# Performance work log

Measured on AMD Instinct MI355X. Metric: run time of the kernel, lower is better.

## Reference

```python
import jax, jax.numpy as jnp
import numpy as np

B, N, S = 8, 4096, 1024
D1, D2 = 128, 256
IN_CH, OUT_CH = D1 + D2, 256
BN_EPS = 1e-5


def setup_inputs() -> dict:
    key = jax.random.key(0)
    ks = jax.random.split(key, 12)
    inp = {
        "xyz1": jax.random.normal(ks[0], (B, N, 3), jnp.float32),
        "xyz2": jax.random.normal(ks[1], (B, S, 3), jnp.float32),
        "points1": jax.random.normal(ks[2], (B, N, D1), jnp.float32),
        "points2": jax.random.normal(ks[3], (B, S, D2), jnp.float32),
        # fuse: Conv1d(in_ch->out_ch, k=1) + BN
        "W_fuse": jax.random.normal(ks[4], (OUT_CH, IN_CH), jnp.float32) * (1.0 / np.sqrt(IN_CH)),
        "b_fuse": jnp.zeros((OUT_CH,), jnp.float32),
        "g_fuse": jnp.ones((OUT_CH,), jnp.float32),
        "bt_fuse": jnp.zeros((OUT_CH,), jnp.float32),
        # res block net1: Conv1d(out_ch->out_ch) + BN (res_expansion=1.0)
        "W1": jax.random.normal(ks[5], (OUT_CH, OUT_CH), jnp.float32) * (1.0 / np.sqrt(OUT_CH)),
        "b1": jnp.zeros((OUT_CH,), jnp.float32),
        "g1": jnp.ones((OUT_CH,), jnp.float32),
        "bt1": jnp.zeros((OUT_CH,), jnp.float32),
        # res block net2: Conv1d(out_ch->out_ch) + BN
        "W2": jax.random.normal(ks[6], (OUT_CH, OUT_CH), jnp.float32) * (1.0 / np.sqrt(OUT_CH)),
        "b2": jnp.zeros((OUT_CH,), jnp.float32),
        "g2": jnp.ones((OUT_CH,), jnp.float32),
        "bt2": jnp.zeros((OUT_CH,), jnp.float32),
    }
    return inp


def _bn(x, g, b):
    # BatchNorm1d training-mode forward: stats over (batch, length), x: [B, C, L]
    m = jnp.mean(x, axis=(0, 2), keepdims=True)
    v = jnp.var(x, axis=(0, 2), keepdims=True)
    return (x - m) * jax.lax.rsqrt(v + BN_EPS) * g[None, :, None] + b[None, :, None]


def _conv1x1(x, W, b):
    # x: [B, C_in, L], W: [C_out, C_in] -> [B, C_out, L]
    return jnp.einsum("oc,bcl->bol", W, x) + b[None, :, None]


def _gelu(x):
    return jax.nn.gelu(x, approximate=False)  # torch nn.GELU default (erf)


def reference(xyz1, xyz2, points1, points2,
              W_fuse, b_fuse, g_fuse, bt_fuse,
              W1, b1, g1, bt1, W2, b2, g2, bt2):
    # squared pairwise distances [B, N, S] without B x N x S x 3 intermediate
    d = (jnp.sum(xyz1 * xyz1, -1)[:, :, None]
         - 2.0 * jnp.einsum("bnc,bsc->bns", xyz1, xyz2)
         + jnp.sum(xyz2 * xyz2, -1)[:, None, :])
    # 3 nearest coarse points per dense point (== sort ascending, take first 3)
    neg_d3, idx = jax.lax.top_k(-d, 3)            # [B, N, 3]
    d3 = -neg_d3
    recip = 1.0 / (d3 + 1e-8)
    w = recip / jnp.sum(recip, axis=2, keepdims=True)  # [B, N, 3]
    gathered = points2[jnp.arange(points2.shape[0])[:, None, None], idx]  # [B, N, 3, D2]
    interp = jnp.sum(gathered * w[..., None], axis=2)  # [B, N, D2]

    new_points = jnp.concatenate([points1, interp], axis=-1)  # [B, N, D1+D2]
    x = jnp.transpose(new_points, (0, 2, 1))                   # [B, C, N]

    # fuse: conv-bn-gelu
    x = _gelu(_bn(_conv1x1(x, W_fuse, b_fuse), g_fuse, bt_fuse))
    # residual block: gelu(bn(conv(gelu(bn(conv(x))))) + x)
    y = _gelu(_bn(_conv1x1(x, W1, b1), g1, bt1))
    y = _bn(_conv1x1(y, W2, b2), g2, bt2)
    x = _gelu(y + x)

    return jnp.transpose(x, (0, 2, 1))  # [B, N, out_ch]
```

## Files before the change

kernel.cpp:

```cpp
#include <hip/hip_runtime.h>
#include <hip/hip_bf16.h>

constexpr int Bb = 8, Nn = 4096, Ss = 1024;
constexpr int D1 = 128, D2 = 256, KIN = 384, OC = 256;
constexpr int L = Bb * Nn;
constexpr float BN_EPS = 1e-5f;

typedef __attribute__((ext_vector_type(4))) float floatx4;
typedef __attribute__((ext_vector_type(8))) __bf16 bf16x8;

#define DEV __device__ __forceinline__

DEV float bf2f(unsigned short u) {
    union { unsigned int i; float f; } v; v.i = ((unsigned int)u) << 16; return v.f;
}
DEV unsigned short f2bf(float f) {
    union { float f; unsigned int i; } v; v.f = f;
    unsigned int x = v.i;
    return (unsigned short)((x + 0x7FFFu + ((x >> 16) & 1u)) >> 16);
}
DEV float gelu_f(float x) {
    float u = x * (0.7978845608f + 0.0356774081f * x * x);
    float t = __expf(-2.0f * u);
    return x * __builtin_amdgcn_rcpf(1.0f + t);
}

DEV bool probe_isf(const unsigned int* __restrict__ w, int tid) {
    unsigned int lo = w[tid & 63] & 0xFFFFu;
    int e = (int)((lo >> 7) & 0xFF);
    unsigned long long m = __ballot(e >= 100 && e <= 144);
    return __popcll(m) < 48;
}

template <int K> DEV int permoff(int off) {
    int row = off / K, rr = off - row * K;
    int cg_ = (rr >> 3) & 7;
    return row * K + (rr & ~63) + (((cg_ ^ (row & 7)) << 3)) + (rr & 7);
}

DEV void merge3(float& d0, float& d1, float& d2, int& i0, int& i1, int& i2,
                float e0, float e1, float e2, int j0, int j1, int j2, bool pref) {
    float a0 = d0, a1 = d1, a2 = d2; int x0 = i0, x1 = i1, x2 = i2;
    float b0 = e0, b1 = e1;          int y0 = j0, y1 = j1;
    bool t = pref ? (a0 <= b0) : (a0 < b0);
    d0 = t ? a0 : b0; i0 = t ? x0 : y0;
    a0 = t ? a1 : a0; x0 = t ? x1 : x0;
    a1 = t ? a2 : a1; x1 = t ? x2 : x1;
    b0 = t ? b0 : b1; y0 = t ? y0 : y1;
    b1 = t ? b1 : e2; y1 = t ? y1 : j2;
    t = pref ? (a0 <= b0) : (a0 < b0);
    d1 = t ? a0 : b0; i1 = t ? x0 : y0;
    a0 = t ? a1 : a0; x0 = t ? x1 : x0;
    b0 = t ? b0 : b1; y0 = t ? y0 : y1;
    t = pref ? (a0 <= b0) : (a0 < b0);
    d2 = t ? a0 : b0; i2 = t ? x0 : y0;
}

__global__ __launch_bounds__(256) void k_front(const void* __restrict__ xyz1_,
                                               const void* __restrict__ xyz2_,
                                               const void* __restrict__ w0_,
                                               const void* __restrict__ w1_,
                                               const void* __restrict__ w2_,
                                               unsigned short* __restrict__ Wdst,
                                               float* __restrict__ stats,
                                               int* __restrict__ dflag,
                                               int* __restrict__ nn_idx,
                                               float* __restrict__ nn_w) {
    int tid = threadIdx.x;
    int bid = blockIdx.x;
    bool isf = probe_isf((const unsigned int*)xyz1_, tid);

    if (bid < 6) {
        stats[bid * 256 + tid] = 0.0f;
        if (bid == 0 && tid == 0) *dflag = isf ? 1 : 0;
        return;
    }
    if (bid < 902) {
        int i = (bid - 6) * 256 + tid;
        const void* src; int off;
        if (i < 98304)       { src = w0_; off = permoff<384>(i); }
        else if (i < 163840) { src = w1_; off = permoff<256>(i - 98304); }
        else                 { src = w2_; off = permoff<256>(i - 163840); }
        Wdst[i] = isf ? f2bf(((const float*)src)[off]) : ((const unsigned short*)src)[off];
        return;
    }

    __shared__ alignas(16) float s4[Ss * 4 + 32];
    int bn0 = (bid - 902) * 32;
    int b = bn0 >> 12;

    if (isf) {
        const float* p2 = (const float*)xyz2_ + (size_t)b * Ss * 3;
        for (int i = tid; i < Ss * 3; i += 256) {
            int s = i / 3, k = i - s * 3;
            s4[s * 4 + k + ((s >> 7) << 2)] = p2[i];
        }
    } else {
        const unsigned short* p2 = (const unsigned short*)xyz2_ + (size_t)b * Ss * 3;
        for (int i = tid; i < Ss * 3; i += 256) {
            int s = i / 3, k = i - s * 3;
            s4[s * 4 + k + ((s >> 7) << 2)] = bf2f(p2[i]);
        }
    }
    __syncthreads();
    for (int s = tid; s < Ss; s += 256) {
        int a = s * 4 + ((s >> 7) << 2);
        float x = s4[a], y = s4[a + 1], z = s4[a + 2];
        s4[a + 3] = x * x + y * y + z * z;
    }
    __syncthreads();

    int part = tid & 7;
    int bn = bn0 + (tid >> 3);
    float x1, y1, z1;
    if (isf) {
        const float* p1 = (const float*)xyz1_ + (size_t)bn * 3;
        x1 = p1[0]; y1 = p1[1]; z1 = p1[2];
    } else {
        const unsigned short* p1 = (const unsigned short*)xyz1_ + (size_t)bn * 3;
        x1 = bf2f(p1[0]); y1 = bf2f(p1[1]); z1 = bf2f(p1[2]);
    }
    float n1 = x1 * x1 + y1 * y1 + z1 * z1;

    float d0 = 3.4e38f, d1 = 3.4e38f, d2 = 3.4e38f;
    int i0 = 0, i1 = 0, i2 = 0;
    const float* sp = &s4[part * 516];
#pragma unroll 4
    for (int j = 0; j < 128; ++j) {
        float4 qv = *(const float4*)(sp + j * 4);
        float d = n1 + qv.w - 2.0f * (x1 * qv.x + y1 * qv.y + z1 * qv.z);
        int s = part * 128 + j;
        bool c2 = d < d2, c1 = d < d1, c0 = d < d0;
        d2 = c1 ? d1 : (c2 ? d : d2); i2 = c1 ? i1 : (c2 ? s : i2);
        d1 = c0 ? d0 : (c1 ? d : d1); i1 = c0 ? i0 : (c1 ? s : i1);
        d0 = c0 ? d  : d0;            i0 = c0 ? s  : i0;
    }
#pragma unroll
    for (int m = 1; m <= 4; m <<= 1) {
        float e0 = __shfl_xor(d0, m, 64), e1 = __shfl_xor(d1, m, 64), e2 = __shfl_xor(d2, m, 64);
        int   j0 = __shfl_xor(i0, m, 64), j1 = __shfl_xor(i1, m, 64), j2 = __shfl_xor(i2, m, 64);
        bool pref = (part < (part ^ m));
        merge3(d0, d1, d2, i0, i1, i2, e0, e1, e2, j0, j1, j2, pref);
    }
    if (part == 0) {
        float r0 = 1.0f / (d0 + 1e-8f), r1 = 1.0f / (d1 + 1e-8f), r2 = 1.0f / (d2 + 1e-8f);
        float rs = 1.0f / (r0 + r1 + r2);
        nn_idx[bn * 3 + 0] = i0; nn_idx[bn * 3 + 1] = i1; nn_idx[bn * 3 + 2] = i2;
        nn_w[bn * 3 + 0] = r0 * rs; nn_w[bn * 3 + 1] = r1 * rs; nn_w[bn * 3 + 2] = r2 * rs;
    }
}

__global__ __launch_bounds__(256) void k_interp(const void* __restrict__ p1_,
                                                const void* __restrict__ p2_,
                                                const int* __restrict__ nn_idx,
                                                const float* __restrict__ nn_w,
                                                const int* __restrict__ dflag,
                                                unsigned short* __restrict__ X) {
    bool isf = (*dflag != 0);
    int i0_ = blockIdx.x * 256 + threadIdx.x;
    constexpr int GPR = KIN / 8;
#pragma unroll
    for (int it = 0; it < 3; ++it) {
        int g = i0_ + it * 524288;
        int row = g / GPR, cg = g - row * GPR;
        int chunk = cg >> 3, cgc = cg & 7;
        union { uint4 v; unsigned short u[8]; } va;
        if (cg < 16) {
            int c0 = cg * 8;
            if (isf) {
                const float* p = (const float*)p1_ + (size_t)row * D1 + c0;
                float4 f0 = *(const float4*)p;
                float4 f1 = *(const float4*)(p + 4);
                va.u[0] = f2bf(f0.x); va.u[1] = f2bf(f0.y); va.u[2] = f2bf(f0.z); va.u[3] = f2bf(f0.w);
                va.u[4] = f2bf(f1.x); va.u[5] = f2bf(f1.y); va.u[6] = f2bf(f1.z); va.u[7] = f2bf(f1.w);
            } else {
                va.v = *(const uint4*)((const unsigned short*)p1_ + (size_t)row * D1 + c0);
            }
        } else {
            int c2 = (cg - 16) * 8;
            int b = row >> 12;
            int j0 = nn_idx[row * 3], j1 = nn_idx[row * 3 + 1], j2 = nn_idx[row * 3 + 2];
            float w0 = nn_w[row * 3], w1 = nn_w[row * 3 + 1], w2 = nn_w[row * 3 + 2];
            if (isf) {
                const float* base = (const float*)p2_;
                const float* r0 = base + ((size_t)(b * Ss + j0)) * D2 + c2;
                const float* r1 = base + ((size_t)(b * Ss + j1)) * D2 + c2;
                const float* r2 = base + ((size_t)(b * Ss + j2)) * D2 + c2;
#pragma unroll
                for (int h = 0; h < 2; ++h) {
                    float4 a0 = *(const float4*)(r0 + h * 4);
                    float4 a1 = *(const float4*)(r1 + h * 4);
                    float4 a2 = *(const float4*)(r2 + h * 4);
                    va.u[h * 4 + 0] = f2bf(w0 * a0.x + w1 * a1.x + w2 * a2.x);
                    va.u[h * 4 + 1] = f2bf(w0 * a0.y + w1 * a1.y + w2 * a2.y);
                    va.u[h * 4 + 2] = f2bf(w0 * a0.z + w1 * a1.z + w2 * a2.z);
                    va.u[h * 4 + 3] = f2bf(w0 * a0.w + w1 * a1.w + w2 * a2.w);
                }
            } else {
                const unsigned short* base = (const unsigned short*)p2_;
                uint4 v0 = *(const uint4*)(base + ((size_t)(b * Ss + j0)) * D2 + c2);
                uint4 v1 = *(const uint4*)(base + ((size_t)(b * Ss + j1)) * D2 + c2);
                uint4 v2 = *(const uint4*)(base + ((size_t)(b * Ss + j2)) * D2 + c2);
                const unsigned short* u0 = (const unsigned short*)&v0;
                const unsigned short* u1 = (const unsigned short*)&v1;
                const unsigned short* u2 = (const unsigned short*)&v2;
#pragma unroll
                for (int j = 0; j < 8; ++j)
                    va.u[j] = f2bf(w0 * bf2f(u0[j]) + w1 * bf2f(u1[j]) + w2 * bf2f(u2[j]));
            }
        }
        *(uint4*)&X[(size_t)row * KIN + chunk * 64 + ((cgc ^ (row & 7)) << 3)] = va.v;
    }
}

template <int K, bool ACT>
__global__ __launch_bounds__(256, 4) void k_gemm(const unsigned short* __restrict__ A,
                                                 const unsigned short* __restrict__ W,
                                                 unsigned short* __restrict__ Out,
                                                 float* __restrict__ S1, float* __restrict__ S2,
                                                 const float* __restrict__ S1in,
                                                 const float* __restrict__ S2in,
                                                 const void* __restrict__ g_,
                                                 const void* __restrict__ bt_,
                                                 const int* __restrict__ dflag) {
    __shared__ alignas(16) unsigned short As[32 * 64];
    __shared__ alignas(16) unsigned short Bs[128 * 64];
    __shared__ float sS1[128], sS2[128];
    __shared__ float sCA[256], sCC[256];

    int tid = threadIdx.x;
    int l0 = (blockIdx.x >> 1) * 32;
    int n0 = (blockIdx.x & 1) * 128;
    int wn = tid >> 6, lane = tid & 63, quad = lane >> 4, lr = lane & 15;

    if constexpr (ACT) {
        float m = S1in[tid] * (1.0f / (float)L);
        float var = S2in[tid] * (1.0f / (float)L) - m * m;
        float g, bt;
        if (*dflag) { g = ((const float*)g_)[tid]; bt = ((const float*)bt_)[tid]; }
        else { g = bf2f(((const unsigned short*)g_)[tid]); bt = bf2f(((const unsigned short*)bt_)[tid]); }
        float a = g * rsqrtf(var + BN_EPS);
        sCA[tid] = a;
        sCC[tid] = bt - m * a;
    }
    if (tid < 128) { sS1[tid] = 0.f; sS2[tid] = 0.f; }

    floatx4 acc[2][2];
#pragma unroll
    for (int mi = 0; mi < 2; ++mi)
#pragma unroll
        for (int ni = 0; ni < 2; ++ni) acc[mi][ni] = (floatx4){0.f, 0.f, 0.f, 0.f};

    for (int kc = 0; kc < K / 64; ++kc) {
        __syncthreads();
#pragma unroll
        for (int it = 0; it < 4; ++it) {
            int chunk = it * 4 + wn;
            int row = chunk * 8 + (lane >> 3);
            const unsigned short* src = W + (size_t)(n0 + row) * K + kc * 64 + (lane & 7) * 8;
            __builtin_amdgcn_global_load_lds(
                (const __attribute__((address_space(1))) void*)src,
                (__attribute__((address_space(3))) void*)&Bs[chunk * 512],
                16, 0, 0);
        }
        if constexpr (!ACT) {
            const unsigned short* src = A + (size_t)(l0 + wn * 8 + (lane >> 3)) * K + kc * 64 + (lane & 7) * 8;
            __builtin_amdgcn_global_load_lds(
                (const __attribute__((address_space(1))) void*)src,
                (__attribute__((address_space(3))) void*)&As[wn * 512],
                16, 0, 0);
        } else {
            int row = tid >> 3, c8 = tid & 7;
            union { uint4 v; unsigned short u[8]; } va;
            va.v = *(const uint4*)(A + (size_t)(l0 + row) * K + kc * 64 + c8 * 8);
            int kb = kc * 64 + c8 * 8;
#pragma unroll
            for (int j = 0; j < 8; ++j) {
                float f = bf2f(va.u[j]);
                va.u[j] = f2bf(gelu_f(sCA[kb + j] * f + sCC[kb + j]));
            }
            *(uint4*)&As[row * 64 + ((c8 ^ (row & 7)) << 3)] = va.v;
        }
        __syncthreads();
#pragma unroll
        for (int ks8 = 0; ks8 < 2; ++ks8) {
            bf16x8 af[2], bfr[2];
#pragma unroll
            for (int mi = 0; mi < 2; ++mi) {
                int ra = mi * 16 + lr;
                af[mi] = *(const bf16x8*)&As[ra * 64 + ((((ks8 << 2) + quad) ^ (ra & 7)) << 3)];
            }
#pragma unroll
            for (int ni = 0; ni < 2; ++ni) {
                int rb = wn * 32 + ni * 16 + lr;
                bfr[ni] = *(const bf16x8*)&Bs[rb * 64 + ((((ks8 << 2) + quad) ^ (rb & 7)) << 3)];
            }
#pragma unroll
            for (int mi = 0; mi < 2; ++mi)
#pragma unroll
                for (int ni = 0; ni < 2; ++ni)
                    acc[mi][ni] = __builtin_amdgcn_mfma_f32_16x16x32_bf16(af[mi], bfr[ni], acc[mi][ni], 0, 0, 0);
        }
    }

    float p1a[2] = {0, 0}, p2a[2] = {0, 0};
#pragma unroll
    for (int mi = 0; mi < 2; ++mi)
#pragma unroll
        for (int ni = 0; ni < 2; ++ni)
#pragma unroll
            for (int r = 0; r < 4; ++r) {
                float v = acc[mi][ni][r];
                int row = l0 + mi * 16 + quad * 4 + r;
                int col = n0 + wn * 32 + ni * 16 + lr;
                Out[(size_t)row * OC + col] = f2bf(v);
                p1a[ni] += v; p2a[ni] += v * v;
            }
    __syncthreads();
#pragma unroll
    for (int ni = 0; ni < 2; ++ni) {
        atomicAdd(&sS1[wn * 32 + ni * 16 + lr], p1a[ni]);
        atomicAdd(&sS2[wn * 32 + ni * 16 + lr], p2a[ni]);
    }
    __syncthreads();
    if (tid < 128) {
        atomicAdd(&S1[n0 + tid], sS1[tid]);
        atomicAdd(&S2[n0 + tid], sS2[tid]);
    }
}

__global__ __launch_bounds__(256) void k_final(const unsigned short* __restrict__ t0,
                                               const unsigned short* __restrict__ t2,
                                               const float* __restrict__ S1_0, const float* __restrict__ S2_0,
                                               const float* __restrict__ S1_2, const float* __restrict__ S2_2,
                                               const void* __restrict__ g0_, const void* __restrict__ bt0_,
                                               const void* __restrict__ g2_, const void* __restrict__ bt2_,
                                               const int* __restrict__ dflag,
                                               void* __restrict__ out_) {
    __shared__ float sA0[256], sC0[256], sA2[256], sC2[256];
    int tid = threadIdx.x;
    bool isf = (*dflag != 0);
    {
        float m0 = S1_0[tid] * (1.0f / (float)L);
        float v0_ = S2_0[tid] * (1.0f / (float)L) - m0 * m0;
        float m2 = S1_2[tid] * (1.0f / (float)L);
        float v2_ = S2_2[tid] * (1.0f / (float)L) - m2 * m2;
        float g0, b0, g2, b2;
        if (isf) {
            g0 = ((const float*)g0_)[tid]; b0 = ((const float*)bt0_)[tid];
            g2 = ((const float*)g2_)[tid]; b2 = ((const float*)bt2_)[tid];
        } else {
            g0 = bf2f(((const unsigned short*)g0_)[tid]); b0 = bf2f(((const unsigned short*)bt0_)[tid]);
            g2 = bf2f(((const unsigned short*)g2_)[tid]); b2 = bf2f(((const unsigned short*)bt2_)[tid]);
        }
        float a0 = g0 * rsqrtf(v0_ + BN_EPS);
        float a2 = g2 * rsqrtf(v2_ + BN_EPS);
        sA0[tid] = a0; sC0[tid] = b0 - m0 * a0;
        sA2[tid] = a2; sC2[tid] = b2 - m2 * a2;
    }
    __syncthreads();

    int idx = (blockIdx.x * 256 + tid) * 8;
    int col = idx & (OC - 1);
    union { uint4 v; unsigned short u[8]; } v0, v2;
    v0.v = *(const uint4*)(t0 + idx);
    v2.v = *(const uint4*)(t2 + idx);
    float r[8];
#pragma unroll
    for (int j = 0; j < 8; ++j) {
        float x = gelu_f(sA0[col + j] * bf2f(v0.u[j]) + sC0[col + j]);
        float y = sA2[col + j] * bf2f(v2.u[j]) + sC2[col + j];
        r[j] = gelu_f(x + y);
    }
    if (isf) {
        float* o = (float*)out_ + idx;
        float4 lo = {r[0], r[1], r[2], r[3]};
        float4 hi = {r[4], r[5], r[6], r[7]};
        *(float4*)o = lo;
        *(float4*)(o + 4) = hi;
    } else {
        union { uint4 v; unsigned short u[8]; } vo;
#pragma unroll
        for (int j = 0; j < 8; ++j) vo.u[j] = f2bf(r[j]);
        *(uint4*)((unsigned short*)out_ + idx) = vo.v;
    }
}

extern "C" void kernel_launch(void* const* d_in, const int* in_sizes, int n_in,
                              void* d_out, int out_size, void* d_ws, size_t ws_size,
                              hipStream_t stream) {
    const void* xyz1    = d_in[0];
    const void* xyz2    = d_in[1];
    const void* points1 = d_in[2];
    const void* points2 = d_in[3];
    const void* W_fuse  = d_in[4];
    const void* g_fuse  = d_in[6];
    const void* bt_fuse = d_in[7];
    const void* W1      = d_in[8];
    const void* g1      = d_in[10];
    const void* bt1     = d_in[11];
    const void* W2      = d_in[12];
    const void* g2      = d_in[14];
    const void* bt2     = d_in[15];

    char* ws = (char*)d_ws;
    unsigned short* t2 = (unsigned short*)ws;
    unsigned short* t0 = (unsigned short*)(ws + 25165824);
    unsigned short* X  = (unsigned short*)d_out;
    unsigned short* t1 = (unsigned short*)d_out;
    int*   nn_idx = (int*)(ws + 41943040);
    float* nn_w   = (float*)(ws + 42336256);
    float* stats  = (float*)(ws + 42729472);
    int*   dflag  = (int*)(ws + 42729472 + 3072 * 4);
    unsigned short* Wbf = (unsigned short*)(ws + 42745856);

    float *S1_0 = stats,        *S2_0 = stats + 256;
    float *S1_1 = stats + 512,  *S2_1 = stats + 768;
    float *S1_2 = stats + 1024, *S2_2 = stats + 1280;

    k_front<<<1926, 256, 0, stream>>>(xyz1, xyz2, W_fuse, W1, W2, Wbf, stats, dflag, nn_idx, nn_w);
    k_interp<<<2048, 256, 0, stream>>>(points1, points2, nn_idx, nn_w, dflag, X);
    k_gemm<KIN, false><<<2048, 256, 0, stream>>>(X, Wbf, t0, S1_0, S2_0,
                                                 nullptr, nullptr, nullptr, nullptr, dflag);
    k_gemm<OC, true><<<2048, 256, 0, stream>>>(t0, Wbf + 98304, t1, S1_1, S2_1,
                                               S1_0, S2_0, g_fuse, bt_fuse, dflag);
    k_gemm<OC, true><<<2048, 256, 0, stream>>>(t1, Wbf + 163840, t2, S1_2, S2_2,
                                               S1_1, S2_1, g1, bt1, dflag);
    k_final<<<L * OC / (256 * 8), 256, 0, stream>>>(t0, t2, S1_0, S2_0, S1_2, S2_2,
                                                    g_fuse, bt_fuse, g2, bt2, dflag, d_out);
}
```

Before: 272.1 us.

## Replace LDS-tiled fused GEMM with register-weight GEMM and separate activation kernels

```diff
diff --git a/kernel.cpp b/kernel.cpp
--- a/kernel.cpp
+++ b/kernel.cpp
@@ -30,12 +30,6 @@
     int e = (int)((lo >> 7) & 0xFF);
     unsigned long long m = __ballot(e >= 100 && e <= 144);
     return __popcll(m) < 48;
-}
-
-template <int K> DEV int permoff(int off) {
-    int row = off / K, rr = off - row * K;
-    int cg_ = (rr >> 3) & 7;
-    return row * K + (rr & ~63) + (((cg_ ^ (row & 7)) << 3)) + (rr & 7);
 }
 
 DEV void merge3(float& d0, float& d1, float& d2, int& i0, int& i1, int& i2,
@@ -78,9 +72,9 @@
     if (bid < 902) {
         int i = (bid - 6) * 256 + tid;
         const void* src; int off;
-        if (i < 98304)       { src = w0_; off = permoff<384>(i); }
-        else if (i < 163840) { src = w1_; off = permoff<256>(i - 98304); }
-        else                 { src = w2_; off = permoff<256>(i - 163840); }
+        if (i < 98304)       { src = w0_; off = i; }
+        else if (i < 163840) { src = w1_; off = i - 98304; }
+        else                 { src = w2_; off = i - 163840; }
         Wdst[i] = isf ? f2bf(((const float*)src)[off]) : ((const unsigned short*)src)[off];
         return;
     }
@@ -163,7 +157,6 @@
     for (int it = 0; it < 3; ++it) {
         int g = i0_ + it * 524288;
         int row = g / GPR, cg = g - row * GPR;
-        int chunk = cg >> 3, cgc = cg & 7;
         union { uint4 v; unsigned short u[8]; } va;
         if (cg < 16) {
             int c0 = cg * 8;
@@ -209,31 +202,70 @@
                     va.u[j] = f2bf(w0 * bf2f(u0[j]) + w1 * bf2f(u1[j]) + w2 * bf2f(u2[j]));
             }
         }
-        *(uint4*)&X[(size_t)row * KIN + chunk * 64 + ((cgc ^ (row & 7)) << 3)] = va.v;
-    }
-}
-
-template <int K, bool ACT>
-__global__ __launch_bounds__(256, 4) void k_gemm(const unsigned short* __restrict__ A,
-                                                 const unsigned short* __restrict__ W,
-                                                 unsigned short* __restrict__ Out,
-                                                 float* __restrict__ S1, float* __restrict__ S2,
-                                                 const float* __restrict__ S1in,
-                                                 const float* __restrict__ S2in,
-                                                 const void* __restrict__ g_,
-                                                 const void* __restrict__ bt_,
-                                                 const int* __restrict__ dflag) {
-    __shared__ alignas(16) unsigned short As[32 * 64];
-    __shared__ alignas(16) unsigned short Bs[128 * 64];
-    __shared__ float sS1[128], sS2[128];
+        *(uint4*)&X[(size_t)row * KIN + cg * 8] = va.v;
+    }
+}
+
+template <int K>
+__global__ __launch_bounds__(256) void k_rgemm(const unsigned short* __restrict__ A,
+                                               const unsigned short* __restrict__ W,
+                                               unsigned short* __restrict__ Out,
+                                               float* __restrict__ S1,
+                                               float* __restrict__ S2) {
+    constexpr int KS = K / 32;
+    int tid = threadIdx.x;
+    int wn = tid >> 6, lane = tid & 63, quad = lane >> 4, lr = lane & 15;
+    int c0 = (((blockIdx.x & 1) << 2) | wn) * 32;
+    int r0 = (blockIdx.x >> 1) * 128;
+
+    bf16x8 bfrag[2][KS];
+#pragma unroll
+    for (int ni = 0; ni < 2; ++ni)
+#pragma unroll
+        for (int ks = 0; ks < KS; ++ks)
+            bfrag[ni][ks] = *(const bf16x8*)&W[(size_t)(c0 + ni * 16 + lr) * K + ks * 32 + quad * 8];
+
+    float p1[2] = {0.f, 0.f}, p2[2] = {0.f, 0.f};
+#pragma unroll 2
+    for (int ch = 0; ch < 8; ++ch) {
+        const unsigned short* arow = A + (size_t)(r0 + ch * 16 + lr) * K + quad * 8;
+        bf16x8 af[KS];
+#pragma unroll
+        for (int ks = 0; ks < KS; ++ks)
+            af[ks] = *(const bf16x8*)(arow + ks * 32);
+        floatx4 acc0 = (floatx4){0.f, 0.f, 0.f, 0.f};
+        floatx4 acc1 = (floatx4){0.f, 0.f, 0.f, 0.f};
+#pragma unroll
+        for (int ks = 0; ks < KS; ++ks) {
+            acc0 = __builtin_amdgcn_mfma_f32_16x16x32_bf16(af[ks], bfrag[0][ks], acc0, 0, 0, 0);
+            acc1 = __builtin_amdgcn_mfma_f32_16x16x32_bf16(af[ks], bfrag[1][ks], acc1, 0, 0, 0);
+        }
+        int orow = r0 + ch * 16 + quad * 4;
+#pragma unroll
+        for (int r = 0; r < 4; ++r) {
+            float v0 = acc0[r], v1 = acc1[r];
+            Out[(size_t)(orow + r) * OC + c0 + lr]      = f2bf(v0);
+            Out[(size_t)(orow + r) * OC + c0 + 16 + lr] = f2bf(v1);
+            p1[0] += v0; p2[0] += v0 * v0;
+            p1[1] += v1; p2[1] += v1 * v1;
+        }
+    }
+    atomicAdd(&S1[c0 + lr],      p1[0]);
+    atomicAdd(&S2[c0 + lr],      p2[0]);
+    atomicAdd(&S1[c0 + 16 + lr], p1[1]);
+    atomicAdd(&S2[c0 + 16 + lr], p2[1]);
+}
+
+__global__ __launch_bounds__(256) void k_act(const unsigned short* __restrict__ Tin,
+                                             unsigned short* __restrict__ Tout,
+                                             const float* __restrict__ S1in,
+                                             const float* __restrict__ S2in,
+                                             const void* __restrict__ g_,
+                                             const void* __restrict__ bt_,
+                                             const int* __restrict__ dflag) {
     __shared__ float sCA[256], sCC[256];
-
     int tid = threadIdx.x;
-    int l0 = (blockIdx.x >> 1) * 32;
-    int n0 = (blockIdx.x & 1) * 128;
-    int wn = tid >> 6, lane = tid & 63, quad = lane >> 4, lr = lane & 15;
-
-    if constexpr (ACT) {
+    {
         float m = S1in[tid] * (1.0f / (float)L);
         float var = S2in[tid] * (1.0f / (float)L) - m * m;
         float g, bt;
@@ -243,90 +275,16 @@
         sCA[tid] = a;
         sCC[tid] = bt - m * a;
     }
-    if (tid < 128) { sS1[tid] = 0.f; sS2[tid] = 0.f; }
-
-    floatx4 acc[2][2];
-#pragma unroll
-    for (int mi = 0; mi < 2; ++mi)
-#pragma unroll
-        for (int ni = 0; ni < 2; ++ni) acc[mi][ni] = (floatx4){0.f, 0.f, 0.f, 0.f};
-
-    for (int kc = 0; kc < K / 64; ++kc) {
-        __syncthreads();
-#pragma unroll
-        for (int it = 0; it < 4; ++it) {
-            int chunk = it * 4 + wn;
-            int row = chunk * 8 + (lane >> 3);
-            const unsigned short* src = W + (size_t)(n0 + row) * K + kc * 64 + (lane & 7) * 8;
-            __builtin_amdgcn_global_load_lds(
-                (const __attribute__((address_space(1))) void*)src,
-                (__attribute__((address_space(3))) void*)&Bs[chunk * 512],
-                16, 0, 0);
-        }
-        if constexpr (!ACT) {
-            const unsigned short* src = A + (size_t)(l0 + wn * 8 + (lane >> 3)) * K + kc * 64 + (lane & 7) * 8;
-            __builtin_amdgcn_global_load_lds(
-                (const __attribute__((address_space(1))) void*)src,
-                (__attribute__((address_space(3))) void*)&As[wn * 512],
-                16, 0, 0);
-        } else {
-            int row = tid >> 3, c8 = tid & 7;
-            union { uint4 v; unsigned short u[8]; } va;
-            va.v = *(const uint4*)(A + (size_t)(l0 + row) * K + kc * 64 + c8 * 8);
-            int kb = kc * 64 + c8 * 8;
-#pragma unroll
-            for (int j = 0; j < 8; ++j) {
-                float f = bf2f(va.u[j]);
-                va.u[j] = f2bf(gelu_f(sCA[kb + j] * f + sCC[kb + j]));
-            }
-            *(uint4*)&As[row * 64 + ((c8 ^ (row & 7)) << 3)] = va.v;
-        }
-        __syncthreads();
-#pragma unroll
-        for (int ks8 = 0; ks8 < 2; ++ks8) {
-            bf16x8 af[2], bfr[2];
-#pragma unroll
-            for (int mi = 0; mi < 2; ++mi) {
-                int ra = mi * 16 + lr;
-                af[mi] = *(const bf16x8*)&As[ra * 64 + ((((ks8 << 2) + quad) ^ (ra & 7)) << 3)];
-            }
-#pragma unroll
-            for (int ni = 0; ni < 2; ++ni) {
-                int rb = wn * 32 + ni * 16 + lr;
-                bfr[ni] = *(const bf16x8*)&Bs[rb * 64 + ((((ks8 << 2) + quad) ^ (rb & 7)) << 3)];
-            }
-#pragma unroll
-            for (int mi = 0; mi < 2; ++mi)
-#pragma unroll
-                for (int ni = 0; ni < 2; ++ni)
-                    acc[mi][ni] = __builtin_amdgcn_mfma_f32_16x16x32_bf16(af[mi], bfr[ni], acc[mi][ni], 0, 0, 0);
-        }
-    }
-
-    float p1a[2] = {0, 0}, p2a[2] = {0, 0};
-#pragma unroll
-    for (int mi = 0; mi < 2; ++mi)
-#pragma unroll
-        for (int ni = 0; ni < 2; ++ni)
-#pragma unroll
-            for (int r = 0; r < 4; ++r) {
-                float v = acc[mi][ni][r];
-                int row = l0 + mi * 16 + quad * 4 + r;
-                int col = n0 + wn * 32 + ni * 16 + lr;
-                Out[(size_t)row * OC + col] = f2bf(v);
-                p1a[ni] += v; p2a[ni] += v * v;
-            }
     __syncthreads();
-#pragma unroll
-    for (int ni = 0; ni < 2; ++ni) {
-        atomicAdd(&sS1[wn * 32 + ni * 16 + lr], p1a[ni]);
-        atomicAdd(&sS2[wn * 32 + ni * 16 + lr], p2a[ni]);
-    }
-    __syncthreads();
-    if (tid < 128) {
-        atomicAdd(&S1[n0 + tid], sS1[tid]);
-        atomicAdd(&S2[n0 + tid], sS2[tid]);
-    }
+
+    int idx = (blockIdx.x * 256 + tid) * 8;
+    int col = idx & (OC - 1);
+    union { uint4 v; unsigned short u[8]; } vi, vo;
+    vi.v = *(const uint4*)(Tin + idx);
+#pragma unroll
+    for (int j = 0; j < 8; ++j)
+        vo.u[j] = f2bf(gelu_f(sCA[col + j] * bf2f(vi.u[j]) + sCC[col + j]));
+    *(uint4*)(Tout + idx) = vo.v;
 }
 
 __global__ __launch_bounds__(256) void k_final(const unsigned short* __restrict__ t0,
@@ -404,15 +362,16 @@
     const void* bt2     = d_in[15];
 
     char* ws = (char*)d_ws;
-    unsigned short* t2 = (unsigned short*)ws;
-    unsigned short* t0 = (unsigned short*)(ws + 25165824);
+    unsigned short* t0 = (unsigned short*)ws;
+    unsigned short* t2 = (unsigned short*)(ws + 16777216);
+    unsigned short* ta = (unsigned short*)(ws + 33554432);
     unsigned short* X  = (unsigned short*)d_out;
     unsigned short* t1 = (unsigned short*)d_out;
-    int*   nn_idx = (int*)(ws + 41943040);
-    float* nn_w   = (float*)(ws + 42336256);
-    float* stats  = (float*)(ws + 42729472);
-    int*   dflag  = (int*)(ws + 42729472 + 3072 * 4);
-    unsigned short* Wbf = (unsigned short*)(ws + 42745856);
+    int*   nn_idx = (int*)(ws + 50331648);
+    float* nn_w   = (float*)(ws + 50724864);
+    float* stats  = (float*)(ws + 51118080);
+    int*   dflag  = (int*)(ws + 51124224);
+    unsigned short* Wbf = (unsigned short*)(ws + 51126272);
 
     float *S1_0 = stats,        *S2_0 = stats + 256;
     float *S1_1 = stats + 512,  *S2_1 = stats + 768;
@@ -420,12 +379,11 @@
 
     k_front<<<1926, 256, 0, stream>>>(xyz1, xyz2, W_fuse, W1, W2, Wbf, stats, dflag, nn_idx, nn_w);
     k_interp<<<2048, 256, 0, stream>>>(points1, points2, nn_idx, nn_w, dflag, X);
-    k_gemm<KIN, false><<<2048, 256, 0, stream>>>(X, Wbf, t0, S1_0, S2_0,
-                                                 nullptr, nullptr, nullptr, nullptr, dflag);
-    k_gemm<OC, true><<<2048, 256, 0, stream>>>(t0, Wbf + 98304, t1, S1_1, S2_1,
-                                               S1_0, S2_0, g_fuse, bt_fuse, dflag);
-    k_gemm<OC, true><<<2048, 256, 0, stream>>>(t1, Wbf + 163840, t2, S1_2, S2_2,
-                                               S1_1, S2_1, g1, bt1, dflag);
+    k_rgemm<KIN><<<512, 256, 0, stream>>>(X, Wbf, t0, S1_0, S2_0);
+    k_act<<<L * OC / (256 * 8), 256, 0, stream>>>(t0, ta, S1_0, S2_0, g_fuse, bt_fuse, dflag);
+    k_rgemm<OC><<<512, 256, 0, stream>>>(ta, Wbf + 98304, t1, S1_1, S2_1);
+    k_act<<<L * OC / (256 * 8), 256, 0, stream>>>(t1, ta, S1_1, S2_1, g1, bt1, dflag);
+    k_rgemm<OC><<<512, 256, 0, stream>>>(ta, Wbf + 163840, t2, S1_2, S2_2);
     k_final<<<L * OC / (256 * 8), 256, 0, stream>>>(t0, t2, S1_0, S2_0, S1_2, S2_2,
                                                     g_fuse, bt_fuse, g2, bt2, dflag, d_out);
 }
```

Result: slower. 502.1 us (+84.6%).

## Split BN-GELU into separate pass and keep whole weight slice resident in LDS

Applied to the files above, without the earlier changes.

```diff
diff --git a/kernel.cpp b/kernel.cpp
--- a/kernel.cpp
+++ b/kernel.cpp
@@ -213,27 +213,119 @@
     }
 }
 
-template <int K, bool ACT>
-__global__ __launch_bounds__(256, 4) void k_gemm(const unsigned short* __restrict__ A,
-                                                 const unsigned short* __restrict__ W,
-                                                 unsigned short* __restrict__ Out,
-                                                 float* __restrict__ S1, float* __restrict__ S2,
-                                                 const float* __restrict__ S1in,
-                                                 const float* __restrict__ S2in,
-                                                 const void* __restrict__ g_,
-                                                 const void* __restrict__ bt_,
-                                                 const int* __restrict__ dflag) {
-    __shared__ alignas(16) unsigned short As[32 * 64];
-    __shared__ alignas(16) unsigned short Bs[128 * 64];
-    __shared__ float sS1[128], sS2[128];
+template <int K, int BN>
+__global__ __launch_bounds__(256) void k_pgemm(const unsigned short* __restrict__ A,
+                                               const unsigned short* __restrict__ W,
+                                               unsigned short* __restrict__ Out,
+                                               float* __restrict__ S1,
+                                               float* __restrict__ S2) {
+    constexpr int NSPLIT = OC / BN;
+    constexpr int NI = BN / 32;
+    constexpr int WITERS = BN * K / (8 * 256);
+    constexpr int NKC = K / 64;
+
+    __shared__ alignas(16) unsigned short Ws[BN * K];
+    __shared__ alignas(16) unsigned short As[64 * 64];
+    __shared__ float sS1[BN], sS2[BN];
+
+    int tid = threadIdx.x;
+    int n0 = (blockIdx.x % NSPLIT) * BN;
+    int m0 = (blockIdx.x / NSPLIT) * 64;
+    int wn = tid >> 6, lane = tid & 63, quad = lane >> 4, lr = lane & 15;
+    int wm = wn >> 1, wc = wn & 1;
+
+#pragma unroll
+    for (int it = 0; it < WITERS; ++it) {
+        int c = it * 4 + wn;
+        int flat = c * 512 + lane * 8;
+        int row = flat / K, col = flat % K;
+        const unsigned short* src = W + (size_t)(n0 + row) * K + col;
+        __builtin_amdgcn_global_load_lds(
+            (const __attribute__((address_space(1))) void*)src,
+            (__attribute__((address_space(3))) void*)&Ws[c * 512],
+            16, 0, 0);
+    }
+    if (tid < BN) { sS1[tid] = 0.f; sS2[tid] = 0.f; }
+
+    floatx4 acc[2][NI];
+#pragma unroll
+    for (int mi = 0; mi < 2; ++mi)
+#pragma unroll
+        for (int ni = 0; ni < NI; ++ni) acc[mi][ni] = (floatx4){0.f, 0.f, 0.f, 0.f};
+
+    for (int kc = 0; kc < NKC; ++kc) {
+        __syncthreads();
+#pragma unroll
+        for (int it = 0; it < 2; ++it) {
+            int c = it * 4 + wn;
+            int flat = c * 512 + lane * 8;
+            int row = flat >> 6, col = flat & 63;
+            const unsigned short* src = A + (size_t)(m0 + row) * K + kc * 64 + col;
+            __builtin_amdgcn_global_load_lds(
+                (const __attribute__((address_space(1))) void*)src,
+                (__attribute__((address_space(3))) void*)&As[c * 512],
+                16, 0, 0);
+        }
+        __syncthreads();
+#pragma unroll
+        for (int ks8 = 0; ks8 < 2; ++ks8) {
+            bf16x8 af[2], bf[NI];
+#pragma unroll
+            for (int mi = 0; mi < 2; ++mi) {
+                int ra = wm * 32 + mi * 16 + lr;
+                af[mi] = *(const bf16x8*)&As[ra * 64 + ((((ks8 << 2) + quad) ^ (ra & 7)) << 3)];
+            }
+#pragma unroll
+            for (int ni = 0; ni < NI; ++ni) {
+                int rb = wc * (BN / 2) + ni * 16 + lr;
+                bf[ni] = *(const bf16x8*)&Ws[rb * K + kc * 64 + ((((ks8 << 2) + quad) ^ (rb & 7)) << 3)];
+            }
+#pragma unroll
+            for (int mi = 0; mi < 2; ++mi)
+#pragma unroll
+                for (int ni = 0; ni < NI; ++ni)
+                    acc[mi][ni] = __builtin_amdgcn_mfma_f32_16x16x32_bf16(af[mi], bf[ni], acc[mi][ni], 0, 0, 0);
+        }
+    }
+
+    float p1a[NI], p2a[NI];
+#pragma unroll
+    for (int ni = 0; ni < NI; ++ni) { p1a[ni] = 0.f; p2a[ni] = 0.f; }
+#pragma unroll
+    for (int mi = 0; mi < 2; ++mi)
+#pragma unroll
+        for (int ni = 0; ni < NI; ++ni)
+#pragma unroll
+            for (int r = 0; r < 4; ++r) {
+                float v = acc[mi][ni][r];
+                int row = m0 + wm * 32 + mi * 16 + quad * 4 + r;
+                int col = n0 + wc * (BN / 2) + ni * 16 + lr;
+                Out[(size_t)row * OC + col] = f2bf(v);
+                p1a[ni] += v; p2a[ni] += v * v;
+            }
+    __syncthreads();
+#pragma unroll
+    for (int ni = 0; ni < NI; ++ni) {
+        atomicAdd(&sS1[wc * (BN / 2) + ni * 16 + lr], p1a[ni]);
+        atomicAdd(&sS2[wc * (BN / 2) + ni * 16 + lr], p2a[ni]);
+    }
+    __syncthreads();
+    if (tid < BN) {
+        atomicAdd(&S1[n0 + tid], sS1[tid]);
+        atomicAdd(&S2[n0 + tid], sS2[tid]);
+    }
+}
+
+__global__ __launch_bounds__(256) void k_act(const unsigned short* __restrict__ Tin,
+                                             unsigned short* __restrict__ Tout,
+                                             const float* __restrict__ S1in,
+                                             const float* __restrict__ S2in,
+                                             const void* __restrict__ g_,
+                                             const void* __restrict__ bt_,
+                                             const int* __restrict__ dflag) {
     __shared__ float sCA[256], sCC[256];
-
     int tid = threadIdx.x;
-    int l0 = (blockIdx.x >> 1) * 32;
-    int n0 = (blockIdx.x & 1) * 128;
-    int wn = tid >> 6, lane = tid & 63, quad = lane >> 4, lr = lane & 15;
-
-    if constexpr (ACT) {
+    {
         float m = S1in[tid] * (1.0f / (float)L);
         float var = S2in[tid] * (1.0f / (float)L) - m * m;
         float g, bt;
@@ -243,90 +335,19 @@
         sCA[tid] = a;
         sCC[tid] = bt - m * a;
     }
-    if (tid < 128) { sS1[tid] = 0.f; sS2[tid] = 0.f; }
-
-    floatx4 acc[2][2];
-#pragma unroll
-    for (int mi = 0; mi < 2; ++mi)
-#pragma unroll
-        for (int ni = 0; ni < 2; ++ni) acc[mi][ni] = (floatx4){0.f, 0.f, 0.f, 0.f};
-
-    for (int kc = 0; kc < K / 64; ++kc) {
-        __syncthreads();
-#pragma unroll
-        for (int it = 0; it < 4; ++it) {
-            int chunk = it * 4 + wn;
-            int row = chunk * 8 + (lane >> 3);
-            const unsigned short* src = W + (size_t)(n0 + row) * K + kc * 64 + (lane & 7) * 8;
-            __builtin_amdgcn_global_load_lds(
-                (const __attribute__((address_space(1))) void*)src,
-                (__attribute__((address_space(3))) void*)&Bs[chunk * 512],
-                16, 0, 0);
-        }
-        if constexpr (!ACT) {
-            const unsigned short* src = A + (size_t)(l0 + wn * 8 + (lane >> 3)) * K + kc * 64 + (lane & 7) * 8;
-            __builtin_amdgcn_global_load_lds(
-                (const __attribute__((address_space(1))) void*)src,
-                (__attribute__((address_space(3))) void*)&As[wn * 512],
-                16, 0, 0);
-        } else {
-            int row = tid >> 3, c8 = tid & 7;
-            union { uint4 v; unsigned short u[8]; } va;
-            va.v = *(const uint4*)(A + (size_t)(l0 + row) * K + kc * 64 + c8 * 8);
-            int kb = kc * 64 + c8 * 8;
-#pragma unroll
-            for (int j = 0; j < 8; ++j) {
-                float f = bf2f(va.u[j]);
-                va.u[j] = f2bf(gelu_f(sCA[kb + j] * f + sCC[kb + j]));
-            }
-            *(uint4*)&As[row * 64 + ((c8 ^ (row & 7)) << 3)] = va.v;
-        }
-        __syncthreads();
-#pragma unroll
-        for (int ks8 = 0; ks8 < 2; ++ks8) {
-            bf16x8 af[2], bfr[2];
-#pragma unroll
-            for (int mi = 0; mi < 2; ++mi) {
-                int ra = mi * 16 + lr;
-                af[mi] = *(const bf16x8*)&As[ra * 64 + ((((ks8 << 2) + quad) ^ (ra & 7)) << 3)];
-            }
-#pragma unroll
-            for (int ni = 0; ni < 2; ++ni) {
-                int rb = wn * 32 + ni * 16 + lr;
-                bfr[ni] = *(const bf16x8*)&Bs[rb * 64 + ((((ks8 << 2) + quad) ^ (rb & 7)) << 3)];
-            }
-#pragma unroll
-            for (int mi = 0; mi < 2; ++mi)
-#pragma unroll
-                for (int ni = 0; ni < 2; ++ni)
-                    acc[mi][ni] = __builtin_amdgcn_mfma_f32_16x16x32_bf16(af[mi], bfr[ni], acc[mi][ni], 0, 0, 0);
-        }
-    }
-
-    float p1a[2] = {0, 0}, p2a[2] = {0, 0};
-#pragma unroll
-    for (int mi = 0; mi < 2; ++mi)
-#pragma unroll
-        for (int ni = 0; ni < 2; ++ni)
-#pragma unroll
-            for (int r = 0; r < 4; ++r) {
-                float v = acc[mi][ni][r];
-                int row = l0 + mi * 16 + quad * 4 + r;
-                int col = n0 + wn * 32 + ni * 16 + lr;
-                Out[(size_t)row * OC + col] = f2bf(v);
-                p1a[ni] += v; p2a[ni] += v * v;
-            }
-    __syncthreads();
-#pragma unroll
-    for (int ni = 0; ni < 2; ++ni) {
-        atomicAdd(&sS1[wn * 32 + ni * 16 + lr], p1a[ni]);
-        atomicAdd(&sS2[wn * 32 + ni * 16 + lr], p2a[ni]);
-    }
-    __syncthreads();
-    if (tid < 128) {
-        atomicAdd(&S1[n0 + tid], sS1[tid]);
-        atomicAdd(&S2[n0 + tid], sS2[tid]);
-    }
+    __syncthreads();
+
+    int idx = (blockIdx.x * 256 + tid) * 8;
+    int row = idx >> 8;
+    int cg = (idx & 255) >> 3;
+    int col = idx & (OC - 1);
+    union { uint4 v; unsigned short u[8]; } vi, vo;
+    vi.v = *(const uint4*)(Tin + idx);
+#pragma unroll
+    for (int j = 0; j < 8; ++j)
+        vo.u[j] = f2bf(gelu_f(sCA[col + j] * bf2f(vi.u[j]) + sCC[col + j]));
+    int sg = (cg & 24) | ((cg & 7) ^ (row & 7));
+    *(uint4*)(Tout + (size_t)row * OC + sg * 8) = vo.v;
 }
 
 __global__ __launch_bounds__(256) void k_final(const unsigned short* __restrict__ t0,
@@ -404,15 +425,16 @@
     const void* bt2     = d_in[15];
 
     char* ws = (char*)d_ws;
-    unsigned short* t2 = (unsigned short*)ws;
-    unsigned short* t0 = (unsigned short*)(ws + 25165824);
+    unsigned short* t0 = (unsigned short*)ws;
+    unsigned short* t2 = (unsigned short*)(ws + 16777216);
+    unsigned short* ta = (unsigned short*)(ws + 33554432);
     unsigned short* X  = (unsigned short*)d_out;
     unsigned short* t1 = (unsigned short*)d_out;
-    int*   nn_idx = (int*)(ws + 41943040);
-    float* nn_w   = (float*)(ws + 42336256);
-    float* stats  = (float*)(ws + 42729472);
-    int*   dflag  = (int*)(ws + 42729472 + 3072 * 4);
-    unsigned short* Wbf = (unsigned short*)(ws + 42745856);
+    int*   nn_idx = (int*)(ws + 50331648);
+    float* nn_w   = (float*)(ws + 50724864);
+    float* stats  = (float*)(ws + 51118080);
+    int*   dflag  = (int*)(ws + 51124224);
+    unsigned short* Wbf = (unsigned short*)(ws + 51126272);
 
     float *S1_0 = stats,        *S2_0 = stats + 256;
     float *S1_1 = stats + 512,  *S2_1 = stats + 768;
@@ -420,12 +442,11 @@
 
     k_front<<<1926, 256, 0, stream>>>(xyz1, xyz2, W_fuse, W1, W2, Wbf, stats, dflag, nn_idx, nn_w);
     k_interp<<<2048, 256, 0, stream>>>(points1, points2, nn_idx, nn_w, dflag, X);
-    k_gemm<KIN, false><<<2048, 256, 0, stream>>>(X, Wbf, t0, S1_0, S2_0,
-                                                 nullptr, nullptr, nullptr, nullptr, dflag);
-    k_gemm<OC, true><<<2048, 256, 0, stream>>>(t0, Wbf + 98304, t1, S1_1, S2_1,
-                                               S1_0, S2_0, g_fuse, bt_fuse, dflag);
-    k_gemm<OC, true><<<2048, 256, 0, stream>>>(t1, Wbf + 163840, t2, S1_2, S2_2,
-                                               S1_1, S2_1, g1, bt1, dflag);
+    k_pgemm<KIN, 64><<<(L / 64) * 4, 256, 0, stream>>>(X, Wbf, t0, S1_0, S2_0);
+    k_act<<<L * OC / (256 * 8), 256, 0, stream>>>(t0, ta, S1_0, S2_0, g_fuse, bt_fuse, dflag);
+    k_pgemm<OC, 128><<<(L / 64) * 2, 256, 0, stream>>>(ta, Wbf + 98304, t1, S1_1, S2_1);
+    k_act<<<L * OC / (256 * 8), 256, 0, stream>>>(t1, ta, S1_1, S2_1, g1, bt1, dflag);
+    k_pgemm<OC, 128><<<(L / 64) * 2, 256, 0, stream>>>(ta, Wbf + 163840, t2, S1_2, S2_2);
     k_final<<<L * OC / (256 * 8), 256, 0, stream>>>(t0, t2, S1_0, S2_0, S1_2, S2_2,
                                                     g_fuse, bt_fuse, g2, bt2, dflag, d_out);
 }
```

Result: faster. 265.6 us (-2.4%).
